# Optimization experiments

Measured on AMD Instinct MI355X. Metric: run time of the kernel, lower is better.

## Reference

```python
import jax, jax.numpy as jnp
import numpy as np

EPS = 1e-5

def _batchnorm(x, gamma, beta):
    # x: [N, C, T]; training-mode BN: batch stats over (N, T) per channel
    mean = jnp.mean(x, axis=(0, 2), keepdims=True)
    var = jnp.mean((x - mean) ** 2, axis=(0, 2), keepdims=True)
    xhat = (x - mean) * jax.lax.rsqrt(var + EPS)
    return xhat * gamma[None, :, None] + beta[None, :, None]

def _temporal_shift(x, s):
    # x: [N, C, T], s: [C] learnable per-channel shift (Shift-GCN style)
    # out[n,c,t] = linear interp of x[n,c, t + s[c]], zero outside [0, T)
    N, C, T = x.shape
    pos = jnp.arange(T, dtype=x.dtype)[None, :] + s[:, None]  # [C, T]
    i0f = jnp.floor(pos)
    frac = pos - i0f                                          # [C, T]
    i0 = i0f.astype(jnp.int32)
    i1 = i0 + 1
    v0 = ((i0 >= 0) & (i0 < T)).astype(x.dtype)
    v1 = ((i1 >= 0) & (i1 < T)).astype(x.dtype)
    cidx = jnp.arange(C)[:, None]                             # [C, 1]
    g0 = x[:, cidx, jnp.clip(i0, 0, T - 1)]                   # [N, C, T]
    g1 = x[:, cidx, jnp.clip(i1, 0, T - 1)]
    return g0 * ((1.0 - frac) * v0) + g1 * (frac * v1)

def setup_inputs() -> dict:
    key = jax.random.key(0)
    ks = jax.random.split(key, 5)
    N, T, Cin, Cout = 128, 1024, 256, 256
    x = jax.random.normal(ks[0], (N, T, Cin), dtype=jnp.float32)
    # kaiming_normal fan_out for 1x1 conv: std = sqrt(2 / Cout)
    conv_w = jax.random.normal(ks[1], (Cout, Cin), dtype=jnp.float32) * np.sqrt(2.0 / Cout)
    conv_b = jnp.zeros((Cout,), dtype=jnp.float32)
    shift_in_s = jax.random.uniform(ks[2], (Cin,), dtype=jnp.float32, minval=-1.0, maxval=1.0)
    shift_out_s = jax.random.uniform(ks[3], (Cout,), dtype=jnp.float32, minval=-1.0, maxval=1.0)
    return {
        "x": x,
        "bn1_gamma": jnp.ones((Cin,), jnp.float32),
        "bn1_beta": jnp.zeros((Cin,), jnp.float32),
        "shift_in_s": shift_in_s,
        "conv_w": conv_w,
        "conv_b": conv_b,
        "shift_out_s": shift_out_s,
        "bn2_gamma": jnp.ones((Cout,), jnp.float32),
        "bn2_beta": jnp.zeros((Cout,), jnp.float32),
    }

def reference(x, bn1_gamma, bn1_beta, shift_in_s, conv_w, conv_b, shift_out_s, bn2_gamma, bn2_beta):
    # x: [N, T, C] -> [N, C, T] (permute; trailing singleton W dim elided)
    h = jnp.transpose(x, (0, 2, 1))
    h = _batchnorm(h, bn1_gamma, bn1_beta)
    h = _temporal_shift(h, shift_in_s)
    # 1x1 conv == per-position channel mixing
    h = jnp.einsum("nct,oc->not", h, conv_w) + conv_b[None, :, None]
    h = jax.nn.relu(h)
    h = _temporal_shift(h, shift_out_s)
    h = _batchnorm(h, bn2_gamma, bn2_beta)
    return jnp.transpose(h, (0, 2, 1))  # back to [N, T, C_out]
```

## Files before the change

### kernel.cpp

```cpp
#include <hip/hip_runtime.h>
#include <stddef.h>

typedef __attribute__((ext_vector_type(8))) short short8;
typedef __attribute__((ext_vector_type(4))) float f32x4;
typedef __attribute__((ext_vector_type(4))) int   i32x4;
typedef __attribute__((ext_vector_type(2))) unsigned int u32x2;
typedef unsigned short ushort_t;
typedef unsigned int uint_t;

#define NN 128
#define TT 1024
#define CC 256
#define NT 131072.0f
#define EPS 1e-5f
#define LDE 260

__device__ __forceinline__ float bf2f(ushort_t u){
    union { float f; uint_t i; } v; v.i = ((uint_t)u) << 16; return v.f;
}
__device__ __forceinline__ ushort_t f2bf(float f){
    union { float f; uint_t i; } v; v.f = f;
    uint_t r = v.i + 0x7fffu + ((v.i >> 16) & 1u);
    return (ushort_t)(r >> 16);
}
__device__ __forceinline__ uint_t pack2(float lo, float hi){
    return (uint_t)f2bf(lo) | ((uint_t)f2bf(hi) << 16);
}
__device__ __forceinline__ f32x4 ld4bf(const ushort_t* p){
    u32x2 u = *(const u32x2*)p;
    f32x4 r;
    r[0] = bf2f((ushort_t)(u[0] & 0xffffu));
    r[1] = bf2f((ushort_t)(u[0] >> 16));
    r[2] = bf2f((ushort_t)(u[1] & 0xffffu));
    r[3] = bf2f((ushort_t)(u[1] >> 16));
    return r;
}
__device__ __forceinline__ void wave_red(float& v){
    #pragma unroll
    for (int off = 32; off > 0; off >>= 1) v += __shfl_down(v, off);
}

__global__ __launch_bounds__(256) void k_stats1(const float* __restrict__ x,
                                                float* __restrict__ psum,
                                                float* __restrict__ psq){
    __shared__ float ls[4][256], lq[4][256];
    const int b = blockIdx.x, tid = threadIdx.x;
    const int c4 = (tid & 63) << 2, rq = tid >> 6;
    const float* p = x + ((size_t)b << 16) + ((size_t)(rq * 64) << 8) + c4;
    f32x4 s = {0.f,0.f,0.f,0.f}, q = {0.f,0.f,0.f,0.f};
    #pragma unroll 8
    for (int k = 0; k < 64; ++k){
        f32x4 v = *(const f32x4*)&p[(size_t)k << 8];
        #pragma unroll
        for (int j = 0; j < 4; ++j){ s[j] += v[j]; q[j] = fmaf(v[j], v[j], q[j]); }
    }
    #pragma unroll
    for (int j = 0; j < 4; ++j){ ls[rq][c4 + j] = s[j]; lq[rq][c4 + j] = q[j]; }
    __syncthreads();
    const int c = tid;
    psum[c * 512 + b] = ls[0][c] + ls[1][c] + ls[2][c] + ls[3][c];
    psq [c * 512 + b] = lq[0][c] + lq[1][c] + lq[2][c] + lq[3][c];
}

__global__ __launch_bounds__(256) void k_fin1(const float* __restrict__ psum,
                                              const float* __restrict__ psq,
                                              const float* __restrict__ g1,
                                              const float* __restrict__ be1,
                                              const float* __restrict__ sin_,
                                              const float* __restrict__ sout,
                                              float* __restrict__ s1, float* __restrict__ b1,
                                              float* __restrict__ a0i, float* __restrict__ a1i,
                                              int* __restrict__ i1i,
                                              float* __restrict__ a0o, float* __restrict__ a1o,
                                              int* __restrict__ j1o){
    const int c = blockIdx.x, t = threadIdx.x;
    float s = psum[c * 512 + t] + psum[c * 512 + 256 + t];
    float q = psq [c * 512 + t] + psq [c * 512 + 256 + t];
    wave_red(s); wave_red(q);
    __shared__ float sm[8];
    const int wv = t >> 6, ln = t & 63;
    if (ln == 0){ sm[wv] = s; sm[4 + wv] = q; }
    __syncthreads();
    if (t == 0){
        float S = sm[0] + sm[1] + sm[2] + sm[3];
        float Q = sm[4] + sm[5] + sm[6] + sm[7];
        float mean = S / NT;
        float var  = Q / NT - mean * mean;
        float rstd = rsqrtf(var + EPS);
        float sc = rstd * g1[c];
        s1[c] = sc;
        b1[c] = be1[c] - mean * sc;
        float sv = sin_[c]; float fi = floorf(sv); float fr = sv - fi;
        a0i[c] = 1.f - fr; a1i[c] = fr; i1i[c] = (int)fi + 1;
        float so = sout[c]; float fo = floorf(so); float fro = so - fo;
        a0o[c] = 1.f - fro; a1o[c] = fro; j1o[c] = (int)fo + 1;
    }
}

__global__ __launch_bounds__(256) void k_wf(const float* __restrict__ W, ushort_t* __restrict__ WF){
    const int gid = blockIdx.x * 256 + threadIdx.x;
    const int l = gid & 63, ob = (gid >> 6) & 15, ks = gid >> 10;
    const int row = ob * 16 + (l & 15);
    const int k0  = ks * 32 + (l >> 4) * 8;
    #pragma unroll
    for (int j = 0; j < 8; ++j)
        WF[(size_t)gid * 8 + j] = f2bf(W[(size_t)row * 256 + k0 + j]);
}

__device__ __forceinline__ f32x4 bload(const float* xb, int g, f32x4 s, f32x4 b){
    f32x4 r = {0.f,0.f,0.f,0.f};
    if (g >= 0 && g < TT){
        f32x4 xv = *(const f32x4*)&xb[(size_t)g << 8];
        #pragma unroll
        for (int j = 0; j < 4; ++j) r[j] = fmaf(xv[j], s[j], b[j]);
    }
    return r;
}

__global__ __launch_bounds__(256) void k_conv(const float* __restrict__ x,
                                              const ushort_t* __restrict__ WF,
                                              const float* __restrict__ cb,
                                              const float* __restrict__ s1,
                                              const float* __restrict__ b1,
                                              const float* __restrict__ a0i,
                                              const float* __restrict__ a1i,
                                              const int* __restrict__ i1i,
                                              ushort_t* __restrict__ Y){
    __shared__ __align__(16) ushort_t lds[16640];
    const int tid = threadIdx.x;
    const int n  = blockIdx.x >> 4;
    const int t0 = (blockIdx.x & 15) << 6;
    const int lane = tid & 63, wv = tid >> 6;

    {
        const int c4 = lane << 2;
        const f32x4 s1v = *(const f32x4*)&s1[c4];
        const f32x4 b1v = *(const f32x4*)&b1[c4];
        const f32x4 a0v = *(const f32x4*)&a0i[c4];
        const f32x4 a1v = *(const f32x4*)&a1i[c4];
        const i32x4 i1v = *(const i32x4*)&i1i[c4];
        const float* xb = x + ((size_t)n << 18) + c4;
        const int rt = t0 + (wv << 4);
        f32x4 Bm1 = bload(xb, rt - 1, s1v, b1v);
        f32x4 B0  = bload(xb, rt,     s1v, b1v);
        #pragma unroll 4
        for (int k = 0; k < 16; ++k){
            f32x4 Bp1 = bload(xb, rt + k + 1, s1v, b1v);
            f32x4 v;
            #pragma unroll
            for (int j = 0; j < 4; ++j){
                float zl = i1v[j] ? B0[j]  : Bm1[j];
                float zr = i1v[j] ? Bp1[j] : B0[j];
                v[j] = a0v[j] * zl + a1v[j] * zr;
            }
            const int tw = (wv << 4) + k;
            u32x2 w; w[0] = pack2(v[0], v[1]); w[1] = pack2(v[2], v[3]);
            *(u32x2*)&lds[(tw << 8) + (c4 ^ ((tw & 7) << 3))] = w;
            Bm1 = B0; B0 = Bp1;
        }
    }
    __syncthreads();

    const int l15 = lane & 15, lg = lane >> 4;
    f32x4 acc[4][4];
    #pragma unroll
    for (int r = 0; r < 4; ++r)
        #pragma unroll
        for (int q = 0; q < 4; ++q)
            acc[r][q] = (f32x4){0.f, 0.f, 0.f, 0.f};

    const short8* wf8 = (const short8*)WF;
    #pragma unroll
    for (int ks = 0; ks < 8; ++ks){
        short8 aF[4], bF[4];
        #pragma unroll
        for (int r = 0; r < 4; ++r)
            aF[r] = wf8[(ks * 16 + wv * 4 + r) * 64 + lane];
        const int kk = (ks << 5) + (lg << 3);
        #pragma unroll
        for (int q = 0; q < 4; ++q){
            const int t = (q << 4) | l15;
            bF[q] = *(const short8*)&lds[(t << 8) + (kk ^ ((t & 7) << 3))];
        }
        #pragma unroll
        for (int r = 0; r < 4; ++r)
            #pragma unroll
            for (int q = 0; q < 4; ++q)
                acc[r][q] = __builtin_amdgcn_mfma_f32_16x16x32_bf16(aF[r], bF[q], acc[r][q], 0, 0, 0);
    }
    __syncthreads();

    #pragma unroll
    for (int r = 0; r < 4; ++r){
        const int ob = (wv << 6) + (r << 4) + (lg << 2);
        const f32x4 cbv = *(const f32x4*)&cb[ob];
        #pragma unroll
        for (int q = 0; q < 4; ++q){
            const int t = (q << 4) | l15;
            float v[4];
            #pragma unroll
            for (int j = 0; j < 4; ++j){
                float z = acc[r][q][j] + cbv[j];
                v[j] = z > 0.f ? z : 0.f;
            }
            u32x2 w; w[0] = pack2(v[0], v[1]); w[1] = pack2(v[2], v[3]);
            *(u32x2*)&lds[t * LDE + ob] = w;
        }
    }
    __syncthreads();

    u32x2* Yu = (u32x2*)Y;
    const size_t rbase = ((size_t)n << 10) + t0;
    #pragma unroll
    for (int it = 0; it < 16; ++it){
        const int row = (it << 2) + wv;
        u32x2 v = *(const u32x2*)&lds[row * LDE + (lane << 2)];
        Yu[((rbase + row) << 6) + lane] = v;
    }
}

__global__ __launch_bounds__(256) void k_zstats(const ushort_t* __restrict__ Y,
                                                float* __restrict__ ZP, float* __restrict__ ZQ,
                                                float* __restrict__ ZR,
                                                float* __restrict__ B0p, float* __restrict__ B0q,
                                                float* __restrict__ BTp, float* __restrict__ BTq){
    __shared__ float lp[4][256], lq[4][256], lr[4][256];
    const int b = blockIdx.x, tid = threadIdx.x;
    const int n = b >> 2, o4 = (tid & 63) << 2, rq = tid >> 6;
    const int rs = ((b & 3) << 8) + (rq << 6);
    const ushort_t* yb = Y + ((size_t)n << 18) + o4;
    f32x4 P = {0.f,0.f,0.f,0.f}, Q = P, R = P;
    f32x4 prev = {0.f,0.f,0.f,0.f};
    if (rs > 0) prev = ld4bf(yb + ((size_t)(rs - 1) << 8));
    #pragma unroll 8
    for (int k = 0; k < 64; ++k){
        f32x4 y = ld4bf(yb + ((size_t)(rs + k) << 8));
        #pragma unroll
        for (int j = 0; j < 4; ++j){
            P[j] += y[j];
            Q[j] = fmaf(y[j], y[j], Q[j]);
            R[j] = fmaf(prev[j], y[j], R[j]);
        }
        prev = y;
    }
    #pragma unroll
    for (int j = 0; j < 4; ++j){
        lp[rq][o4 + j] = P[j]; lq[rq][o4 + j] = Q[j]; lr[rq][o4 + j] = R[j];
    }
    __syncthreads();
    const int o = tid;
    ZP[o * 512 + b] = lp[0][o] + lp[1][o] + lp[2][o] + lp[3][o];
    ZQ[o * 512 + b] = lq[0][o] + lq[1][o] + lq[2][o] + lq[3][o];
    ZR[o * 512 + b] = lr[0][o] + lr[1][o] + lr[2][o] + lr[3][o];
    if (((b & 3) == 0) && rq == 0){
        f32x4 y0 = ld4bf(yb);
        #pragma unroll
        for (int j = 0; j < 4; ++j){
            B0p[(o4 + j) * 128 + n] = y0[j];
            B0q[(o4 + j) * 128 + n] = y0[j] * y0[j];
        }
    }
    if (((b & 3) == 3) && rq == 3){
        f32x4 yT = ld4bf(yb + ((size_t)1023 << 8));
        #pragma unroll
        for (int j = 0; j < 4; ++j){
            BTp[(o4 + j) * 128 + n] = yT[j];
            BTq[(o4 + j) * 128 + n] = yT[j] * yT[j];
        }
    }
}

__global__ __launch_bounds__(256) void k_fin2(const float* __restrict__ ZP,
                                              const float* __restrict__ ZQ,
                                              const float* __restrict__ ZR,
                                              const float* __restrict__ B0p,
                                              const float* __restrict__ B0q,
                                              const float* __restrict__ BTp,
                                              const float* __restrict__ BTq,
                                              const float* __restrict__ g2,
                                              const float* __restrict__ be2,
                                              const float* __restrict__ a0o,
                                              const float* __restrict__ a1o,
                                              const int* __restrict__ j1o,
                                              float* __restrict__ s2, float* __restrict__ b2){
    const int o = blockIdx.x, t = threadIdx.x;
    float P = ZP[o * 512 + t] + ZP[o * 512 + 256 + t];
    float Q = ZQ[o * 512 + t] + ZQ[o * 512 + 256 + t];
    float R = ZR[o * 512 + t] + ZR[o * 512 + 256 + t];
    float b0 = 0.f, b0s = 0.f, btv = 0.f, bts = 0.f;
    if (t < 128){
        b0 = B0p[o * 128 + t]; b0s = B0q[o * 128 + t];
        btv = BTp[o * 128 + t]; bts = BTq[o * 128 + t];
    }
    wave_red(P); wave_red(Q); wave_red(R);
    wave_red(b0); wave_red(b0s); wave_red(btv); wave_red(bts);
    __shared__ float sm[4][7];
    const int wv = t >> 6, ln = t & 63;
    if (ln == 0){
        sm[wv][0] = P; sm[wv][1] = Q; sm[wv][2] = R;
        sm[wv][3] = b0; sm[wv][4] = b0s; sm[wv][5] = btv; sm[wv][6] = bts;
    }
    __syncthreads();
    if (t == 0){
        float v[7];
        #pragma unroll
        for (int k = 0; k < 7; ++k)
            v[k] = sm[0][k] + sm[1][k] + sm[2][k] + sm[3][k];
        const float a0 = a0o[o], a1 = a1o[o];
        const int j1 = j1o[o];
        float sz, sq;
        if (j1 == 0){
            sz = a0 * (v[0] - v[5]) + a1 * v[0];
            sq = a0 * a0 * (v[1] - v[6]) + a1 * a1 * v[1] + 2.f * a0 * a1 * v[2];
        } else {
            sz = a0 * v[0] + a1 * (v[0] - v[3]);
            sq = a0 * a0 * v[1] + a1 * a1 * (v[1] - v[4]) + 2.f * a0 * a1 * v[2];
        }
        float mean = sz / NT;
        float var  = sq / NT - mean * mean;
        float rstd = rsqrtf(var + EPS);
        float sc = rstd * g2[o];
        s2[o] = sc;
        b2[o] = be2[o] - mean * sc;
    }
}

__global__ __launch_bounds__(256) void k_out(const ushort_t* __restrict__ Y,
                                             const float* __restrict__ s2,
                                             const float* __restrict__ b2,
                                             const float* __restrict__ a0o,
                                             const float* __restrict__ a1o,
                                             const int* __restrict__ j1o,
                                             float* __restrict__ out){
    const int b = blockIdx.x, tid = threadIdx.x;
    const int n = b >> 2, o4 = (tid & 63) << 2, rq = tid >> 6;
    const int rs = ((b & 3) << 8) + (rq << 6);
    const f32x4 sc = *(const f32x4*)&s2[o4];
    const f32x4 bs = *(const f32x4*)&b2[o4];
    const f32x4 a0 = *(const f32x4*)&a0o[o4];
    const f32x4 a1 = *(const f32x4*)&a1o[o4];
    const i32x4 j1 = *(const i32x4*)&j1o[o4];
    const ushort_t* yb = Y + ((size_t)n << 18) + o4;
    float* ob = out + ((size_t)n << 18) + o4;
    f32x4 ym1 = {0.f,0.f,0.f,0.f};
    if (rs > 0) ym1 = ld4bf(yb + ((size_t)(rs - 1) << 8));
    f32x4 y0 = ld4bf(yb + ((size_t)rs << 8));
    #pragma unroll 8
    for (int k = 0; k < 64; ++k){
        const int t = rs + k;
        f32x4 yp1 = {0.f,0.f,0.f,0.f};
        if (t < 1023) yp1 = ld4bf(yb + ((size_t)(t + 1) << 8));
        f32x4 ov;
        #pragma unroll
        for (int j = 0; j < 4; ++j){
            float zl = j1[j] ? y0[j]  : ym1[j];
            float zr = j1[j] ? yp1[j] : y0[j];
            float z = a0[j] * zl + a1[j] * zr;
            ov[j] = fmaf(z, sc[j], bs[j]);
        }
        *(f32x4*)&ob[(size_t)t << 8] = ov;
        ym1 = y0; y0 = yp1;
    }
}

extern "C" void kernel_launch(void* const* d_in, const int* in_sizes, int n_in,
                              void* d_out, int out_size, void* d_ws, size_t ws_size,
                              hipStream_t stream){
    const float* x    = (const float*)d_in[0];
    const float* g1   = (const float*)d_in[1];
    const float* be1  = (const float*)d_in[2];
    const float* sin_ = (const float*)d_in[3];
    const float* W    = (const float*)d_in[4];
    const float* cb   = (const float*)d_in[5];
    const float* sout = (const float*)d_in[6];
    const float* g2   = (const float*)d_in[7];
    const float* be2  = (const float*)d_in[8];
    float* out = (float*)d_out;

    char* ws = (char*)d_ws;
    ushort_t* Y  = (ushort_t*)ws;
    ushort_t* WF = (ushort_t*)(ws + 67108864);
    float* par = (float*)(ws + 67239936);
    float* s1  = par;          float* b1  = par + 256;
    float* a0i = par + 512;    float* a1i = par + 768;
    int*   i1i = (int*)(par + 1024);
    float* a0o = par + 1280;   float* a1o = par + 1536;
    int*   j1o = (int*)(par + 1792);
    float* s2  = par + 2048;   float* b2  = par + 2304;
    float* psum = par + 2560;
    float* psq  = psum + 131072;
    float* ZP   = psq  + 131072;
    float* ZQ   = ZP   + 131072;
    float* ZR   = ZQ   + 131072;
    float* B0p  = ZR   + 131072;
    float* B0q  = B0p  + 32768;
    float* BTp  = B0q  + 32768;
    float* BTq  = BTp  + 32768;

    k_stats1<<<512, 256, 0, stream>>>(x, psum, psq);
    k_fin1  <<<256, 256, 0, stream>>>(psum, psq, g1, be1, sin_, sout,
                                      s1, b1, a0i, a1i, i1i, a0o, a1o, j1o);
    k_wf    <<<32, 256, 0, stream>>>(W, WF);
    k_conv  <<<2048, 256, 0, stream>>>(x, WF, cb, s1, b1, a0i, a1i, i1i, Y);
    k_zstats<<<512, 256, 0, stream>>>(Y, ZP, ZQ, ZR, B0p, B0q, BTp, BTq);
    k_fin2  <<<256, 256, 0, stream>>>(ZP, ZQ, ZR, B0p, B0q, BTp, BTq,
                                      g2, be2, a0o, a1o, j1o, s2, b2);
    k_out   <<<512, 256, 0, stream>>>(Y, s2, b2, a0o, a1o, j1o, out);
}
```

Before: 151.2 us.

## Fold BN1 into conv weights, stage bf16 input, fuse output stats into conv

The stats pass now also writes a bf16 copy of the input into the output buffer, and the conv reads that copy instead of fp32 x. The BN1 scale is folded into the bf16 weights and the shift into a per-channel bias with edge corrections. The second-BN statistics (sum, sum of squares, lag-1 cross term, first/last rows) are computed in the conv epilogue from LDS, which removes the separate zstats pass over Y. Grids for stats and output are also resized and the LDS padding is replaced by an XOR swizzle. The cost is an extra bf16 write of x and more partial-sum traffic, and quantising x to bf16 before normalisation could reduce accuracy.

Result: slower. 168.9 us (+11.7%).

```diff
diff --git a/kernel.cpp b/kernel.cpp
--- a/kernel.cpp
+++ b/kernel.cpp
@@ -8,12 +8,9 @@
 typedef unsigned short ushort_t;
 typedef unsigned int uint_t;
 
-#define NN 128
 #define TT 1024
-#define CC 256
 #define NT 131072.0f
 #define EPS 1e-5f
-#define LDE 260
 
 __device__ __forceinline__ float bf2f(ushort_t u){
     union { float f; uint_t i; } v; v.i = ((uint_t)u) << 16; return v.f;
@@ -41,16 +38,21 @@
 }
 
 __global__ __launch_bounds__(256) void k_stats1(const float* __restrict__ x,
+                                                ushort_t* __restrict__ xb16,
                                                 float* __restrict__ psum,
                                                 float* __restrict__ psq){
     __shared__ float ls[4][256], lq[4][256];
     const int b = blockIdx.x, tid = threadIdx.x;
     const int c4 = (tid & 63) << 2, rq = tid >> 6;
-    const float* p = x + ((size_t)b << 16) + ((size_t)(rq * 64) << 8) + c4;
+    const size_t row0 = ((size_t)b << 6) + ((size_t)rq << 4);
+    const float* p = x + (row0 << 8) + c4;
+    ushort_t* w = xb16 + (row0 << 8) + c4;
     f32x4 s = {0.f,0.f,0.f,0.f}, q = {0.f,0.f,0.f,0.f};
     #pragma unroll 8
-    for (int k = 0; k < 64; ++k){
+    for (int k = 0; k < 16; ++k){
         f32x4 v = *(const f32x4*)&p[(size_t)k << 8];
+        u32x2 u; u[0] = pack2(v[0], v[1]); u[1] = pack2(v[2], v[3]);
+        *(u32x2*)&w[(size_t)k << 8] = u;
         #pragma unroll
         for (int j = 0; j < 4; ++j){ s[j] += v[j]; q[j] = fmaf(v[j], v[j], q[j]); }
     }
@@ -58,8 +60,8 @@
     for (int j = 0; j < 4; ++j){ ls[rq][c4 + j] = s[j]; lq[rq][c4 + j] = q[j]; }
     __syncthreads();
     const int c = tid;
-    psum[c * 512 + b] = ls[0][c] + ls[1][c] + ls[2][c] + ls[3][c];
-    psq [c * 512 + b] = lq[0][c] + lq[1][c] + lq[2][c] + lq[3][c];
+    psum[(size_t)b * 256 + c] = ls[0][c] + ls[1][c] + ls[2][c] + ls[3][c];
+    psq [(size_t)b * 256 + c] = lq[0][c] + lq[1][c] + lq[2][c] + lq[3][c];
 }
 
 __global__ __launch_bounds__(256) void k_fin1(const float* __restrict__ psum,
@@ -74,8 +76,12 @@
                                               float* __restrict__ a0o, float* __restrict__ a1o,
                                               int* __restrict__ j1o){
     const int c = blockIdx.x, t = threadIdx.x;
-    float s = psum[c * 512 + t] + psum[c * 512 + 256 + t];
-    float q = psq [c * 512 + t] + psq [c * 512 + 256 + t];
+    float s = 0.f, q = 0.f;
+    #pragma unroll
+    for (int i = 0; i < 8; ++i){
+        const size_t b = (size_t)(t * 8 + i);
+        s += psum[b * 256 + c]; q += psq[b * 256 + c];
+    }
     wave_red(s); wave_red(q);
     __shared__ float sm[8];
     const int wv = t >> 6, ln = t & 63;
@@ -97,36 +103,63 @@
     }
 }
 
-__global__ __launch_bounds__(256) void k_wf(const float* __restrict__ W, ushort_t* __restrict__ WF){
+__global__ __launch_bounds__(256) void k_wf(const float* __restrict__ W,
+                                            const float* __restrict__ s1,
+                                            ushort_t* __restrict__ WF){
     const int gid = blockIdx.x * 256 + threadIdx.x;
     const int l = gid & 63, ob = (gid >> 6) & 15, ks = gid >> 10;
     const int row = ob * 16 + (l & 15);
     const int k0  = ks * 32 + (l >> 4) * 8;
     #pragma unroll
     for (int j = 0; j < 8; ++j)
-        WF[(size_t)gid * 8 + j] = f2bf(W[(size_t)row * 256 + k0 + j]);
-}
-
-__device__ __forceinline__ f32x4 bload(const float* xb, int g, f32x4 s, f32x4 b){
+        WF[(size_t)gid * 8 + j] = f2bf(W[(size_t)row * 256 + k0 + j] * s1[k0 + j]);
+}
+
+__global__ __launch_bounds__(256) void k_wb(const float* __restrict__ W,
+                                            const float* __restrict__ cb,
+                                            const float* __restrict__ b1,
+                                            const float* __restrict__ a0i,
+                                            const float* __restrict__ a1i,
+                                            const int* __restrict__ i1i,
+                                            float* __restrict__ bias2,
+                                            float* __restrict__ corr0,
+                                            float* __restrict__ corrT){
+    const int o = blockIdx.x, c = threadIdx.x;
+    const float w = W[(size_t)o * 256 + c];
+    float wb = w * b1[c];
+    float c0 = (i1i[c] == 0) ? wb * a0i[c] : 0.f;
+    float cT = (i1i[c] == 1) ? wb * a1i[c] : 0.f;
+    wave_red(wb); wave_red(c0); wave_red(cT);
+    __shared__ float sm[4][3];
+    const int wv = c >> 6, ln = c & 63;
+    if (ln == 0){ sm[wv][0] = wb; sm[wv][1] = c0; sm[wv][2] = cT; }
+    __syncthreads();
+    if (c == 0){
+        bias2[o] = cb[o] + sm[0][0] + sm[1][0] + sm[2][0] + sm[3][0];
+        corr0[o] = sm[0][1] + sm[1][1] + sm[2][1] + sm[3][1];
+        corrT[o] = sm[0][2] + sm[1][2] + sm[2][2] + sm[3][2];
+    }
+}
+
+__device__ __forceinline__ f32x4 bload16(const ushort_t* xp, int g){
     f32x4 r = {0.f,0.f,0.f,0.f};
-    if (g >= 0 && g < TT){
-        f32x4 xv = *(const f32x4*)&xb[(size_t)g << 8];
-        #pragma unroll
-        for (int j = 0; j < 4; ++j) r[j] = fmaf(xv[j], s[j], b[j]);
-    }
+    if (g >= 0 && g < TT) r = ld4bf(xp + ((size_t)g << 8));
     return r;
 }
 
-__global__ __launch_bounds__(256) void k_conv(const float* __restrict__ x,
+__global__ __launch_bounds__(256) void k_conv(const ushort_t* __restrict__ xb,
                                               const ushort_t* __restrict__ WF,
-                                              const float* __restrict__ cb,
-                                              const float* __restrict__ s1,
-                                              const float* __restrict__ b1,
+                                              const float* __restrict__ bias2,
+                                              const float* __restrict__ corr0,
+                                              const float* __restrict__ corrT,
                                               const float* __restrict__ a0i,
                                               const float* __restrict__ a1i,
                                               const int* __restrict__ i1i,
-                                              ushort_t* __restrict__ Y){
-    __shared__ __align__(16) ushort_t lds[16640];
+                                              ushort_t* __restrict__ Y,
+                                              float* __restrict__ SP, float* __restrict__ SQ,
+                                              float* __restrict__ SR,
+                                              float* __restrict__ FR, float* __restrict__ LR){
+    __shared__ __align__(16) ushort_t lds[16384];
     const int tid = threadIdx.x;
     const int n  = blockIdx.x >> 4;
     const int t0 = (blockIdx.x & 15) << 6;
@@ -134,18 +167,16 @@
 
     {
         const int c4 = lane << 2;
-        const f32x4 s1v = *(const f32x4*)&s1[c4];
-        const f32x4 b1v = *(const f32x4*)&b1[c4];
         const f32x4 a0v = *(const f32x4*)&a0i[c4];
         const f32x4 a1v = *(const f32x4*)&a1i[c4];
         const i32x4 i1v = *(const i32x4*)&i1i[c4];
-        const float* xb = x + ((size_t)n << 18) + c4;
+        const ushort_t* xp = xb + ((size_t)n << 18) + c4;
         const int rt = t0 + (wv << 4);
-        f32x4 Bm1 = bload(xb, rt - 1, s1v, b1v);
-        f32x4 B0  = bload(xb, rt,     s1v, b1v);
-        #pragma unroll 4
+        f32x4 Bm1 = bload16(xp, rt - 1);
+        f32x4 B0  = bload16(xp, rt);
+        #pragma unroll 8
         for (int k = 0; k < 16; ++k){
-            f32x4 Bp1 = bload(xb, rt + k + 1, s1v, b1v);
+            f32x4 Bp1 = bload16(xp, rt + k + 1);
             f32x4 v;
             #pragma unroll
             for (int j = 0; j < 4; ++j){
@@ -190,10 +221,14 @@
     }
     __syncthreads();
 
+    const bool isFirst = (t0 == 0), isLast = (t0 == 960);
     #pragma unroll
     for (int r = 0; r < 4; ++r){
         const int ob = (wv << 6) + (r << 4) + (lg << 2);
-        const f32x4 cbv = *(const f32x4*)&cb[ob];
+        const f32x4 cbv = *(const f32x4*)&bias2[ob];
+        f32x4 c0v = {0.f,0.f,0.f,0.f}, cTv = {0.f,0.f,0.f,0.f};
+        if (isFirst) c0v = *(const f32x4*)&corr0[ob];
+        if (isLast)  cTv = *(const f32x4*)&corrT[ob];
         #pragma unroll
         for (int q = 0; q < 4; ++q){
             const int t = (q << 4) | l15;
@@ -201,10 +236,12 @@
             #pragma unroll
             for (int j = 0; j < 4; ++j){
                 float z = acc[r][q][j] + cbv[j];
+                if (isFirst && t == 0)  z -= c0v[j];
+                if (isLast  && t == 63) z -= cTv[j];
                 v[j] = z > 0.f ? z : 0.f;
             }
             u32x2 w; w[0] = pack2(v[0], v[1]); w[1] = pack2(v[2], v[3]);
-            *(u32x2*)&lds[t * LDE + ob] = w;
+            *(u32x2*)&lds[(t << 8) + (ob ^ ((t & 7) << 3))] = w;
         }
     }
     __syncthreads();
@@ -214,69 +251,57 @@
     #pragma unroll
     for (int it = 0; it < 16; ++it){
         const int row = (it << 2) + wv;
-        u32x2 v = *(const u32x2*)&lds[row * LDE + (lane << 2)];
+        u32x2 v = *(const u32x2*)&lds[(row << 8) + ((lane << 2) ^ ((row & 7) << 3))];
         Yu[((rbase + row) << 6) + lane] = v;
     }
-}
-
-__global__ __launch_bounds__(256) void k_zstats(const ushort_t* __restrict__ Y,
-                                                float* __restrict__ ZP, float* __restrict__ ZQ,
-                                                float* __restrict__ ZR,
-                                                float* __restrict__ B0p, float* __restrict__ B0q,
-                                                float* __restrict__ BTp, float* __restrict__ BTq){
-    __shared__ float lp[4][256], lq[4][256], lr[4][256];
-    const int b = blockIdx.x, tid = threadIdx.x;
-    const int n = b >> 2, o4 = (tid & 63) << 2, rq = tid >> 6;
-    const int rs = ((b & 3) << 8) + (rq << 6);
-    const ushort_t* yb = Y + ((size_t)n << 18) + o4;
+    {
+        const int o = tid;
+        FR[(size_t)blockIdx.x * 256 + o] = bf2f(lds[o]);
+        LR[(size_t)blockIdx.x * 256 + o] = bf2f(lds[(63 << 8) + (o ^ 56)]);
+    }
     f32x4 P = {0.f,0.f,0.f,0.f}, Q = P, R = P;
-    f32x4 prev = {0.f,0.f,0.f,0.f};
-    if (rs > 0) prev = ld4bf(yb + ((size_t)(rs - 1) << 8));
-    #pragma unroll 8
-    for (int k = 0; k < 64; ++k){
-        f32x4 y = ld4bf(yb + ((size_t)(rs + k) << 8));
-        #pragma unroll
-        for (int j = 0; j < 4; ++j){
-            P[j] += y[j];
-            Q[j] = fmaf(y[j], y[j], Q[j]);
-            R[j] = fmaf(prev[j], y[j], R[j]);
-        }
-        prev = y;
-    }
-    #pragma unroll
-    for (int j = 0; j < 4; ++j){
-        lp[rq][o4 + j] = P[j]; lq[rq][o4 + j] = Q[j]; lr[rq][o4 + j] = R[j];
-    }
-    __syncthreads();
-    const int o = tid;
-    ZP[o * 512 + b] = lp[0][o] + lp[1][o] + lp[2][o] + lp[3][o];
-    ZQ[o * 512 + b] = lq[0][o] + lq[1][o] + lq[2][o] + lq[3][o];
-    ZR[o * 512 + b] = lr[0][o] + lr[1][o] + lr[2][o] + lr[3][o];
-    if (((b & 3) == 0) && rq == 0){
-        f32x4 y0 = ld4bf(yb);
-        #pragma unroll
-        for (int j = 0; j < 4; ++j){
-            B0p[(o4 + j) * 128 + n] = y0[j];
-            B0q[(o4 + j) * 128 + n] = y0[j] * y0[j];
-        }
-    }
-    if (((b & 3) == 3) && rq == 3){
-        f32x4 yT = ld4bf(yb + ((size_t)1023 << 8));
-        #pragma unroll
-        for (int j = 0; j < 4; ++j){
-            BTp[(o4 + j) * 128 + n] = yT[j];
-            BTq[(o4 + j) * 128 + n] = yT[j] * yT[j];
-        }
-    }
-}
-
-__global__ __launch_bounds__(256) void k_fin2(const float* __restrict__ ZP,
-                                              const float* __restrict__ ZQ,
-                                              const float* __restrict__ ZR,
-                                              const float* __restrict__ B0p,
-                                              const float* __restrict__ B0q,
-                                              const float* __restrict__ BTp,
-                                              const float* __restrict__ BTq,
+    {
+        const int o4 = lane << 2;
+        const int r0 = wv << 4;
+        f32x4 prev = {0.f,0.f,0.f,0.f};
+        if (wv > 0) prev = ld4bf(&lds[((r0 - 1) << 8) + (o4 ^ (((r0 - 1) & 7) << 3))]);
+        #pragma unroll 8
+        for (int k = 0; k < 16; ++k){
+            const int t = r0 + k;
+            f32x4 y = ld4bf(&lds[(t << 8) + (o4 ^ ((t & 7) << 3))]);
+            #pragma unroll
+            for (int j = 0; j < 4; ++j){
+                P[j] += y[j];
+                Q[j] = fmaf(y[j], y[j], Q[j]);
+                R[j] = fmaf(prev[j], y[j], R[j]);
+            }
+            prev = y;
+        }
+    }
+    __syncthreads();
+    float* fl = (float*)lds;
+    {
+        const int o4 = lane << 2;
+        *(f32x4*)&fl[wv * 768 + o4]       = P;
+        *(f32x4*)&fl[wv * 768 + 256 + o4] = Q;
+        *(f32x4*)&fl[wv * 768 + 512 + o4] = R;
+    }
+    __syncthreads();
+    {
+        const int o = tid;
+        float p = fl[o] + fl[768 + o] + fl[1536 + o] + fl[2304 + o];
+        float q = fl[256 + o] + fl[1024 + o] + fl[1792 + o] + fl[2560 + o];
+        float r = fl[512 + o] + fl[1280 + o] + fl[2048 + o] + fl[2816 + o];
+        const size_t idx = (size_t)blockIdx.x * 256 + o;
+        SP[idx] = p; SQ[idx] = q; SR[idx] = r;
+    }
+}
+
+__global__ __launch_bounds__(256) void k_fin2(const float* __restrict__ SP,
+                                              const float* __restrict__ SQ,
+                                              const float* __restrict__ SR,
+                                              const float* __restrict__ FR,
+                                              const float* __restrict__ LR,
                                               const float* __restrict__ g2,
                                               const float* __restrict__ be2,
                                               const float* __restrict__ a0o,
@@ -284,21 +309,27 @@
                                               const int* __restrict__ j1o,
                                               float* __restrict__ s2, float* __restrict__ b2){
     const int o = blockIdx.x, t = threadIdx.x;
-    float P = ZP[o * 512 + t] + ZP[o * 512 + 256 + t];
-    float Q = ZQ[o * 512 + t] + ZQ[o * 512 + 256 + t];
-    float R = ZR[o * 512 + t] + ZR[o * 512 + 256 + t];
-    float b0 = 0.f, b0s = 0.f, btv = 0.f, bts = 0.f;
-    if (t < 128){
-        b0 = B0p[o * 128 + t]; b0s = B0q[o * 128 + t];
-        btv = BTp[o * 128 + t]; bts = BTq[o * 128 + t];
+    float P = 0.f, Q = 0.f, R = 0.f, b0p = 0.f, b0q = 0.f, btp = 0.f, btq = 0.f;
+    #pragma unroll
+    for (int i = 0; i < 8; ++i){
+        const int b = t * 8 + i;
+        const size_t idx = (size_t)b * 256 + o;
+        P += SP[idx]; Q += SQ[idx];
+        float r = SR[idx];
+        const float fr = FR[idx], lr = LR[idx];
+        const int tile = b & 15;
+        if (tile > 0) r = fmaf(LR[idx - 256], fr, r);
+        R += r;
+        if (tile == 0){ b0p += fr; b0q += fr * fr; }
+        if (tile == 15){ btp += lr; btq += lr * lr; }
     }
     wave_red(P); wave_red(Q); wave_red(R);
-    wave_red(b0); wave_red(b0s); wave_red(btv); wave_red(bts);
+    wave_red(b0p); wave_red(b0q); wave_red(btp); wave_red(btq);
     __shared__ float sm[4][7];
     const int wv = t >> 6, ln = t & 63;
     if (ln == 0){
         sm[wv][0] = P; sm[wv][1] = Q; sm[wv][2] = R;
-        sm[wv][3] = b0; sm[wv][4] = b0s; sm[wv][5] = btv; sm[wv][6] = bts;
+        sm[wv][3] = b0p; sm[wv][4] = b0q; sm[wv][5] = btp; sm[wv][6] = btq;
     }
     __syncthreads();
     if (t == 0){
@@ -333,8 +364,8 @@
                                              const int* __restrict__ j1o,
                                              float* __restrict__ out){
     const int b = blockIdx.x, tid = threadIdx.x;
-    const int n = b >> 2, o4 = (tid & 63) << 2, rq = tid >> 6;
-    const int rs = ((b & 3) << 8) + (rq << 6);
+    const int n = b >> 3, o4 = (tid & 63) << 2, rq = tid >> 6;
+    const int rs = ((b & 7) << 7) + (rq << 5);
     const f32x4 sc = *(const f32x4*)&s2[o4];
     const f32x4 bs = *(const f32x4*)&b2[o4];
     const f32x4 a0 = *(const f32x4*)&a0o[o4];
@@ -346,7 +377,7 @@
     if (rs > 0) ym1 = ld4bf(yb + ((size_t)(rs - 1) << 8));
     f32x4 y0 = ld4bf(yb + ((size_t)rs << 8));
     #pragma unroll 8
-    for (int k = 0; k < 64; ++k){
+    for (int k = 0; k < 32; ++k){
         const int t = rs + k;
         f32x4 yp1 = {0.f,0.f,0.f,0.f};
         if (t < 1023) yp1 = ld4bf(yb + ((size_t)(t + 1) << 8));
@@ -380,30 +411,32 @@
     char* ws = (char*)d_ws;
     ushort_t* Y  = (ushort_t*)ws;
     ushort_t* WF = (ushort_t*)(ws + 67108864);
-    float* par = (float*)(ws + 67239936);
-    float* s1  = par;          float* b1  = par + 256;
-    float* a0i = par + 512;    float* a1i = par + 768;
-    int*   i1i = (int*)(par + 1024);
-    float* a0o = par + 1280;   float* a1o = par + 1536;
-    int*   j1o = (int*)(par + 1792);
-    float* s2  = par + 2048;   float* b2  = par + 2304;
-    float* psum = par + 2560;
-    float* psq  = psum + 131072;
-    float* ZP   = psq  + 131072;
-    float* ZQ   = ZP   + 131072;
-    float* ZR   = ZQ   + 131072;
-    float* B0p  = ZR   + 131072;
-    float* B0q  = B0p  + 32768;
-    float* BTp  = B0q  + 32768;
-    float* BTq  = BTp  + 32768;
-
-    k_stats1<<<512, 256, 0, stream>>>(x, psum, psq);
+    float* SP = (float*)(ws + 67239936);
+    float* SQ = SP + 524288;
+    float* SR = SQ + 524288;
+    float* FR = SR + 524288;
+    float* LR = FR + 524288;
+    float* par = LR + 524288;
+    float* s1    = par;         float* b1    = par + 256;
+    float* a0i   = par + 512;   float* a1i   = par + 768;
+    int*   i1i   = (int*)(par + 1024);
+    float* a0o   = par + 1280;  float* a1o   = par + 1536;
+    int*   j1o   = (int*)(par + 1792);
+    float* s2    = par + 2048;  float* b2    = par + 2304;
+    float* bias2 = par + 2560;  float* corr0 = par + 2816;
+    float* corrT = par + 3072;
+    float* psum = (float*)ws;
+    float* psq  = psum + 524288;
+    ushort_t* xb16 = (ushort_t*)d_out;
+
+    k_stats1<<<2048, 256, 0, stream>>>(x, xb16, psum, psq);
     k_fin1  <<<256, 256, 0, stream>>>(psum, psq, g1, be1, sin_, sout,
                                       s1, b1, a0i, a1i, i1i, a0o, a1o, j1o);
-    k_wf    <<<32, 256, 0, stream>>>(W, WF);
-    k_conv  <<<2048, 256, 0, stream>>>(x, WF, cb, s1, b1, a0i, a1i, i1i, Y);
-    k_zstats<<<512, 256, 0, stream>>>(Y, ZP, ZQ, ZR, B0p, B0q, BTp, BTq);
-    k_fin2  <<<256, 256, 0, stream>>>(ZP, ZQ, ZR, B0p, B0q, BTp, BTq,
+    k_wf    <<<32, 256, 0, stream>>>(W, s1, WF);
+    k_wb    <<<256, 256, 0, stream>>>(W, cb, b1, a0i, a1i, i1i, bias2, corr0, corrT);
+    k_conv  <<<2048, 256, 0, stream>>>(xb16, WF, bias2, corr0, corrT,
+                                       a0i, a1i, i1i, Y, SP, SQ, SR, FR, LR);
+    k_fin2  <<<256, 256, 0, stream>>>(SP, SQ, SR, FR, LR,
                                       g2, be2, a0o, a1o, j1o, s2, b2);
-    k_out   <<<512, 256, 0, stream>>>(Y, s2, b2, a0o, a1o, j1o, out);
-}
+    k_out   <<<1024, 256, 0, stream>>>(Y, s2, b2, a0o, a1o, j1o, out);
+}
```
